# Optimization experiments

Hardware: AMD Instinct MI355X
Metric: run time of the kernel (lower is better)

Reference implementation:

```python
import jax, jax.numpy as jnp
import numpy as np

N_HEADS = 16
HEAD_DIM = 64
STRIDE = 32  # default local_attention_ctx used as stride in 'strided' mode


def _strided_fill_mask(n):
    # Faithful to the torch code: positions where (i >= j) and ((i - j) % stride == 0)
    # get mask value 1, and the code does masked_fill_(mask == 1, -inf),
    # i.e. those positions are set to -inf (inverted polarity, replicated as-is).
    i = jnp.arange(n)[:, None]
    j = jnp.arange(n)[None, :]
    return (i >= j) & (((i - j) % STRIDE) == 0)  # [n, n] bool, True -> -inf


def setup_inputs() -> dict:
    key = jax.random.key(0)
    k_x, k_qkv, k_out = jax.random.split(key, 3)
    b, n, c = 2, 2048, 1024
    inner = N_HEADS * HEAD_DIM  # 1024
    x = jax.random.normal(k_x, (b, n, c), dtype=jnp.float32)
    W_qkv = jax.random.normal(k_qkv, (c, 3 * inner), dtype=jnp.float32) * 0.02
    W_out = jax.random.normal(k_out, (inner, c), dtype=jnp.float32) * 0.02
    b_out = jnp.zeros((c,), dtype=jnp.float32)
    return {"x": x, "W_qkv": W_qkv, "W_out": W_out, "b_out": b_out}


def reference(x, W_qkv, W_out, b_out):
    b, n, c = x.shape
    h, hd = N_HEADS, HEAD_DIM
    scale = c ** (-0.5)  # n_embeddings ** -0.5, as in the original

    qkv = x @ W_qkv                              # [b, n, 3*h*hd]
    q, k, v = jnp.split(qkv, 3, axis=-1)
    def to_heads(t):
        return t.reshape(b, n, h, hd).transpose(0, 2, 1, 3)  # [b, h, n, hd]
    q, k, v = to_heads(q), to_heads(k), to_heads(v)

    dots = jnp.einsum('bhid,bhjd->bhij', q, k) * scale       # [b, h, n, n]
    fill = _strided_fill_mask(n)                             # [n, n]
    dots = jnp.where(fill[None, None], -jnp.inf, dots)

    attn = jax.nn.softmax(dots, axis=-1)
    out = jnp.einsum('bhij,bhjd->bhid', attn, v)             # [b, h, n, hd]
    out = out.transpose(0, 2, 1, 3).reshape(b, n, h * hd)    # [b, n, inner]
    out = out @ W_out + b_out                                # dropout: eval/identity
    return out
```

## Files before the change

kernel.cpp:

```cpp
#include <hip/hip_runtime.h>

typedef __attribute__((ext_vector_type(8))) short bf16x8;
typedef __attribute__((ext_vector_type(4))) float f32x4;

#if __has_builtin(__builtin_amdgcn_exp2f)
#define EXP2F(x) __builtin_amdgcn_exp2f(x)
#else
extern "C" __device__ float __ocml_native_exp2_f32(float);
#define EXP2F(x) __ocml_native_exp2_f32(x)
#endif

#define QSCALE 0.04508422002778011f
#define NS 2048

__device__ __forceinline__ ushort f32_to_bf16(float f) {
  union { float f; unsigned u; } x; x.f = f;
  unsigned r = x.u + 0x7fffu + ((x.u >> 16) & 1u);
  return (ushort)(r >> 16);
}

__device__ __forceinline__ unsigned pack_bf16(float f0, float f1) {
#if __has_builtin(__builtin_amdgcn_cvt_pk_bf16_f32)
  auto pr = __builtin_amdgcn_cvt_pk_bf16_f32(f0, f1);
  unsigned u; __builtin_memcpy(&u, &pr, sizeof(u)); return u;
#else
  union { float f; unsigned u; } a, b;
  a.f = f0; b.f = f1;
  return __builtin_amdgcn_perm(b.u + 0x8000u, a.u + 0x8000u, 0x07060302u);
#endif
}

__device__ __forceinline__ void load16_to_lds(const void* g, void* l) {
  __builtin_amdgcn_global_load_lds(
      (const __attribute__((address_space(1))) unsigned int*)(
          reinterpret_cast<uintptr_t>(g)),
      (__attribute__((address_space(3))) unsigned int*)(
          reinterpret_cast<uintptr_t>(l)),
      16, 0, 0);
}

__global__ __launch_bounds__(256) void prep(
    const float* __restrict__ x, const float* __restrict__ Wqkv,
    ushort* __restrict__ xb, ushort* __restrict__ wqkvT)
{
  __shared__ ushort tile[32][33];
  const int bid = blockIdx.x, t = threadIdx.x;
  if (bid < 2048) {
    size_t i = (size_t)bid * 256 + t;
    const float4* p = (const float4*)(x + i * 8);
    float4 a = p[0], b = p[1];
    union { uint4 v; ushort s[8]; } u;
    u.s[0] = f32_to_bf16(a.x); u.s[1] = f32_to_bf16(a.y);
    u.s[2] = f32_to_bf16(a.z); u.s[3] = f32_to_bf16(a.w);
    u.s[4] = f32_to_bf16(b.x); u.s[5] = f32_to_bf16(b.y);
    u.s[6] = f32_to_bf16(b.z); u.s[7] = f32_to_bf16(b.w);
    *(uint4*)(xb + i * 8) = u.v;
  } else {
    int tb = bid - 2048;
    int cb = (tb % 96) * 32, rb = (tb / 96) * 32;
    int tx = t & 31, ty = t >> 5;
    float s = (cb + tx) < 1024 ? QSCALE : 1.0f;
#pragma unroll
    for (int k = 0; k < 4; ++k)
      tile[ty + 8 * k][tx] =
          f32_to_bf16(Wqkv[(size_t)(rb + ty + 8 * k) * 3072 + cb + tx] * s);
    __syncthreads();
#pragma unroll
    for (int k = 0; k < 4; ++k)
      wqkvT[(size_t)(cb + ty + 8 * k) * 1024 + rb + tx] = tile[tx][ty + 8 * k];
  }
}

__global__ __launch_bounds__(256) void transpose_w(
    const float* __restrict__ in, ushort* __restrict__ out, int R, int C)
{
  __shared__ ushort tile[32][33];
  int t = threadIdx.x, tx = t & 31, ty = t >> 5;
  int rb = blockIdx.y * 32, cb = blockIdx.x * 32;
#pragma unroll
  for (int k = 0; k < 4; ++k)
    tile[ty + 8 * k][tx] = f32_to_bf16(in[(size_t)(rb + ty + 8 * k) * C + cb + tx]);
  __syncthreads();
#pragma unroll
  for (int k = 0; k < 4; ++k)
    out[(size_t)(cb + ty + 8 * k) * R + rb + tx] = tile[tx][ty + 8 * k];
}

template <typename TC>
__device__ __forceinline__ void gemm_core(
    const ushort* __restrict__ A, const ushort* __restrict__ Bt,
    const float* __restrict__ bias, TC* __restrict__ C,
    int N, int K, int mbase, int nbase,
    ushort* __restrict__ sA0, ushort* __restrict__ sB0,
    ushort* __restrict__ sA1, ushort* __restrict__ sB1)
{
  const int t = threadIdx.x;
  const int lane = t & 63, w = t >> 6;
  const int quad = lane >> 4, l16 = lane & 15;
  const int wr = w >> 1, wc = w & 1;
  const int lrow = lane >> 2, lchunk = (lane & 3) * 8;

  f32x4 acc[4][4];
#pragma unroll
  for (int i = 0; i < 4; ++i)
#pragma unroll
    for (int j = 0; j < 4; ++j)
      acc[i][j] = (f32x4){0.f, 0.f, 0.f, 0.f};

#pragma unroll
  for (int r = 0; r < 2; ++r) {
    int rb = w * 32 + r * 16;
    load16_to_lds(&A[(size_t)(mbase + rb + lrow) * K + lchunk], &sA0[rb * 32]);
    load16_to_lds(&Bt[(size_t)(nbase + rb + lrow) * K + lchunk], &sB0[rb * 32]);
  }

  for (int kb = 0; kb < K; kb += 32) {
    const bool odd = (kb >> 5) & 1;
    ushort* sA = odd ? sA1 : sA0;
    ushort* sB = odd ? sB1 : sB0;
    ushort* pA = odd ? sA0 : sA1;
    ushort* pB = odd ? sB0 : sB1;
    __syncthreads();
    if (kb + 32 < K) {
#pragma unroll
      for (int r = 0; r < 2; ++r) {
        int rb = w * 32 + r * 16;
        load16_to_lds(&A[(size_t)(mbase + rb + lrow) * K + kb + 32 + lchunk],
                      &pA[rb * 32]);
        load16_to_lds(&Bt[(size_t)(nbase + rb + lrow) * K + kb + 32 + lchunk],
                      &pB[rb * 32]);
      }
    }

    bf16x8 af[4], bf[4];
#pragma unroll
    for (int mt = 0; mt < 4; ++mt)
      af[mt] = *(const bf16x8*)&sA[(wr * 64 + mt * 16 + l16) * 32 + quad * 8];
#pragma unroll
    for (int nt = 0; nt < 4; ++nt)
      bf[nt] = *(const bf16x8*)&sB[(wc * 64 + nt * 16 + l16) * 32 + quad * 8];
#pragma unroll
    for (int mt = 0; mt < 4; ++mt)
#pragma unroll
      for (int nt = 0; nt < 4; ++nt)
        acc[mt][nt] = __builtin_amdgcn_mfma_f32_16x16x32_bf16(
            af[mt], bf[nt], acc[mt][nt], 0, 0, 0);
  }

#pragma unroll
  for (int mt = 0; mt < 4; ++mt) {
#pragma unroll
    for (int nt = 0; nt < 4; ++nt) {
      int col = nbase + wc * 64 + nt * 16 + l16;
      float bv = bias ? bias[col] : 0.f;
#pragma unroll
      for (int ri = 0; ri < 4; ++ri) {
        int row = mbase + wr * 64 + mt * 16 + quad * 4 + ri;
        float val = acc[mt][nt][ri] + bv;
        if constexpr (__is_same(TC, float))
          C[(size_t)row * N + col] = val;
        else
          C[(size_t)row * N + col] = f32_to_bf16(val);
      }
    }
  }
}

__global__ __launch_bounds__(256) void gemm_qkvt(
    const ushort* __restrict__ xb, const ushort* __restrict__ wqkvT,
    ushort* __restrict__ qk, ushort* __restrict__ vtbuf)
{
  __shared__ ushort sA0[128 * 32], sB0[128 * 32];
  __shared__ ushort sA1[128 * 32], sB1[128 * 32];
  const int bid = blockIdx.x;
  if (bid < 512) {
    gemm_core<ushort>(xb, wqkvT, nullptr, qk, 2048, 1024,
                      (bid >> 4) * 128, (bid & 15) * 128, sA0, sB0, sA1, sB1);
  } else {
    const int id = bid - 512;
    gemm_core<ushort>(wqkvT + (size_t)2048 * 1024, xb, nullptr, vtbuf,
                      4096, 1024, (id >> 5) * 128, (id & 31) * 128,
                      sA0, sB0, sA1, sB1);
  }
}

__global__ __launch_bounds__(256) void gemm_out(
    const ushort* __restrict__ attnb, const ushort* __restrict__ woutT,
    const float* __restrict__ bias, float* __restrict__ out)
{
  __shared__ ushort sA0[128 * 32], sB0[128 * 32];
  __shared__ ushort sA1[128 * 32], sB1[128 * 32];
  const int bid = blockIdx.x;
  gemm_core<float>(attnb, woutT, bias, out, 1024, 1024,
                   (bid >> 3) * 128, (bid & 7) * 128, sA0, sB0, sA1, sB1);
}

__device__ __forceinline__ void stage_kv(
    const ushort* __restrict__ qk, const ushort* __restrict__ vt,
    ushort* sKb, ushort* sVb, int b, int h, int kvbase,
    int w, int rowK, int csw)
{
#pragma unroll
  for (int g = 0; g < 2; ++g) {
    int rk = w * 16 + g * 8 + rowK;
    load16_to_lds(&qk[((size_t)(b * NS + kvbase + rk)) * 2048 + 1024 + h * 64 + csw],
                  &sKb[(w * 16 + g * 8) * 64]);
    load16_to_lds(&vt[((size_t)(h * 64 + rk)) * 4096 + b * 2048 + kvbase + csw],
                  &sVb[(w * 16 + g * 8) * 64]);
  }
}

__global__ __launch_bounds__(256) void attn_kernel(
    const ushort* __restrict__ qk, const ushort* __restrict__ vt,
    ushort* __restrict__ attn_out)
{
  __shared__ ushort sK[2][64 * 64];
  __shared__ ushort sV[2][64 * 64];
  __shared__ ushort sPt[4][32][72];

  const int t = threadIdx.x;
  const int lane = t & 63, w = t >> 6;
  const int quad = lane >> 4, l16 = lane & 15;
  const int bh = blockIdx.y, b = bh >> 4, h = bh & 15;
  const int qbase = blockIdx.x * 128;
  const int rowK = lane >> 3;
  const int csw = ((lane & 7) ^ rowK) * 8;
  const int swz = l16 & 7;

  bf16x8 qf[2][2];
#pragma unroll
  for (int is = 0; is < 2; ++is)
#pragma unroll
    for (int c = 0; c < 2; ++c)
      qf[is][c] = *(const bf16x8*)&qk[
          ((size_t)(b * NS + qbase + w * 32 + is * 16 + l16)) * 2048 +
          h * 64 + c * 32 + quad * 8];

  bf16x8 ones;
  { union { bf16x8 v; ushort s[8]; } ou;
#pragma unroll
    for (int i = 0; i < 8; ++i) ou.s[i] = 0x3F80;
    ones = ou.v; }

  unsigned amask[2][4][2];
#pragma unroll
  for (int is = 0; is < 2; ++is)
#pragma unroll
    for (int mt = 0; mt < 4; ++mt)
#pragma unroll
      for (int hf = 0; hf < 2; ++hf) {
        int r0 = hf * 2, r1 = hf * 2 + 1;
        int base = is * 16 + l16 - mt * 16 - quad * 4;
        unsigned m = 0xFFFFFFFFu;
        if (((base - r0) & 31) == 0) m &= 0xFFFF0000u;
        if (((base - r1) & 31) == 0) m &= 0x0000FFFFu;
        amask[is][mt][hf] = m;
      }

  const int ib64 = (qbase + w * 32) >> 6;

  f32x4 oacc[2][4];
#pragma unroll
  for (int is = 0; is < 2; ++is)
#pragma unroll
    for (int dt = 0; dt < 4; ++dt) oacc[is][dt] = (f32x4){0.f, 0.f, 0.f, 0.f};
  f32x4 lsum[2];
  lsum[0] = (f32x4){0.f, 0.f, 0.f, 0.f};
  lsum[1] = (f32x4){0.f, 0.f, 0.f, 0.f};

  stage_kv(qk, vt, sK[0], sV[0], b, h, 0, w, rowK, csw);

  for (int kb = 0; kb < NS / 64; ++kb) {
    const int cur = kb & 1;
    const int kvbase = kb * 64;
    __syncthreads();
    if (kb < NS / 64 - 1)
      stage_kv(qk, vt, sK[cur ^ 1], sV[cur ^ 1], b, h, kvbase + 64, w, rowK, csw);

    const ushort* K = sK[cur];
    const ushort* V = sV[cur];

    f32x4 st[2][4];
#pragma unroll
    for (int is = 0; is < 2; ++is)
#pragma unroll
      for (int mt = 0; mt < 4; ++mt) st[is][mt] = (f32x4){0.f, 0.f, 0.f, 0.f};
#pragma unroll
    for (int mt = 0; mt < 4; ++mt)
#pragma unroll
      for (int c = 0; c < 2; ++c) {
        bf16x8 kf = *(const bf16x8*)&K[(mt * 16 + l16) * 64 +
                                       (((c * 4 + quad) ^ swz) * 8)];
        st[0][mt] = __builtin_amdgcn_mfma_f32_16x16x32_bf16(
            kf, qf[0][c], st[0][mt], 0, 0, 0);
        st[1][mt] = __builtin_amdgcn_mfma_f32_16x16x32_bf16(
            kf, qf[1][c], st[1][mt], 0, 0, 0);
      }

    if (kb < ib64) {
#pragma unroll
      for (int is = 0; is < 2; ++is)
#pragma unroll
        for (int mt = 0; mt < 4; ++mt) {
          unsigned lo = pack_bf16(EXP2F(st[is][mt][0]), EXP2F(st[is][mt][1])) &
                        amask[is][mt][0];
          unsigned hi = pack_bf16(EXP2F(st[is][mt][2]), EXP2F(st[is][mt][3])) &
                        amask[is][mt][1];
          *(uint2*)&sPt[w][is * 16 + l16][mt * 16 + quad * 4] =
              make_uint2(lo, hi);
        }
    } else if (kb > ib64) {
#pragma unroll
      for (int is = 0; is < 2; ++is)
#pragma unroll
        for (int mt = 0; mt < 4; ++mt) {
          unsigned lo = pack_bf16(EXP2F(st[is][mt][0]), EXP2F(st[is][mt][1]));
          unsigned hi = pack_bf16(EXP2F(st[is][mt][2]), EXP2F(st[is][mt][3]));
          *(uint2*)&sPt[w][is * 16 + l16][mt * 16 + quad * 4] =
              make_uint2(lo, hi);
        }
    } else {
#pragma unroll
      for (int is = 0; is < 2; ++is) {
        int irow = qbase + w * 32 + is * 16 + l16;
#pragma unroll
        for (int mt = 0; mt < 4; ++mt) {
          float p[4];
#pragma unroll
          for (int ri = 0; ri < 4; ++ri) {
            int j = kvbase + mt * 16 + quad * 4 + ri;
            p[ri] = EXP2F(st[is][mt][ri]);
            unsigned du = (unsigned)(irow - j);
            if ((du & 0x8000001Fu) == 0u) p[ri] = 0.f;
          }
          unsigned lo = pack_bf16(p[0], p[1]);
          unsigned hi = pack_bf16(p[2], p[3]);
          *(uint2*)&sPt[w][is * 16 + l16][mt * 16 + quad * 4] =
              make_uint2(lo, hi);
        }
      }
    }

#pragma unroll
    for (int c2 = 0; c2 < 2; ++c2) {
      bf16x8 vf[4];
#pragma unroll
      for (int dt = 0; dt < 4; ++dt)
        vf[dt] = *(const bf16x8*)&V[(dt * 16 + l16) * 64 +
                                    (((c2 * 4 + quad) ^ swz) * 8)];
#pragma unroll
      for (int is = 0; is < 2; ++is) {
        bf16x8 pf = *(const bf16x8*)&sPt[w][is * 16 + l16][c2 * 32 + quad * 8];
        lsum[is] = __builtin_amdgcn_mfma_f32_16x16x32_bf16(
            pf, ones, lsum[is], 0, 0, 0);
#pragma unroll
        for (int dt = 0; dt < 4; ++dt)
          oacc[is][dt] = __builtin_amdgcn_mfma_f32_16x16x32_bf16(
              pf, vf[dt], oacc[is][dt], 0, 0, 0);
      }
    }
  }

#pragma unroll
  for (int is = 0; is < 2; ++is)
#pragma unroll
    for (int ri = 0; ri < 4; ++ri) {
      float inv = __builtin_amdgcn_rcpf(lsum[is][ri]);
      int ig = qbase + w * 32 + is * 16 + quad * 4 + ri;
#pragma unroll
      for (int dt = 0; dt < 4; ++dt)
        attn_out[(size_t)(b * NS + ig) * 1024 + h * 64 + dt * 16 + l16] =
            f32_to_bf16(oacc[is][dt][ri] * inv);
    }
}

extern "C" void kernel_launch(void* const* d_in, const int* in_sizes, int n_in,
                              void* d_out, int out_size, void* d_ws, size_t ws_size,
                              hipStream_t stream) {
  const float* x    = (const float*)d_in[0];
  const float* Wqkv = (const float*)d_in[1];
  const float* Wout = (const float*)d_in[2];
  const float* bout = (const float*)d_in[3];
  float* out = (float*)d_out;

  ushort* qk    = (ushort*)d_ws;
  ushort* vt    = qk + (size_t)4096 * 2048;
  ushort* xb    = vt + (size_t)1024 * 4096;
  ushort* wqkvT = xb + (size_t)4096 * 1024;
  ushort* attnb = xb;
  ushort* woutT = wqkvT;

  prep<<<2048 + 3072, 256, 0, stream>>>(x, Wqkv, xb, wqkvT);
  gemm_qkvt<<<768, 256, 0, stream>>>(xb, wqkvT, qk, vt);
  transpose_w<<<dim3(32, 32), 256, 0, stream>>>(Wout, woutT, 1024, 1024);
  attn_kernel<<<dim3(NS / 128, 32), 256, 0, stream>>>(qk, vt, attnb);
  gemm_out<<<256, 256, 0, stream>>>(attnb, woutT, bout, out);
}
```

Measured before the change: 196.1 us.

## Fuse Wout transpose into prep, swizzle GEMM LDS, retile output GEMM

Folds the W_out bf16 transpose into the prep kernel, removing one launch and giving woutT its own workspace slot. Adds an XOR swizzle on the LDS layout in the shared GEMM core to reduce bank conflicts on fragment reads. Retiles the output GEMM to 64x128 tiles with BK=64, launching 512 blocks instead of 256 for better CU fill. It also drops the hardware packed bf16 convert in favour of a perm-based path, which may alter rounding in attention.

Result: faster. 188.3 us (-4.0%).

```diff
diff --git a/kernel.cpp b/kernel.cpp
--- a/kernel.cpp
+++ b/kernel.cpp
@@ -20,14 +20,9 @@
 }
 
 __device__ __forceinline__ unsigned pack_bf16(float f0, float f1) {
-#if __has_builtin(__builtin_amdgcn_cvt_pk_bf16_f32)
-  auto pr = __builtin_amdgcn_cvt_pk_bf16_f32(f0, f1);
-  unsigned u; __builtin_memcpy(&u, &pr, sizeof(u)); return u;
-#else
   union { float f; unsigned u; } a, b;
   a.f = f0; b.f = f1;
   return __builtin_amdgcn_perm(b.u + 0x8000u, a.u + 0x8000u, 0x07060302u);
-#endif
 }
 
 __device__ __forceinline__ void load16_to_lds(const void* g, void* l) {
@@ -41,7 +36,9 @@
 
 __global__ __launch_bounds__(256) void prep(
     const float* __restrict__ x, const float* __restrict__ Wqkv,
-    ushort* __restrict__ xb, ushort* __restrict__ wqkvT)
+    const float* __restrict__ Wout,
+    ushort* __restrict__ xb, ushort* __restrict__ wqkvT,
+    ushort* __restrict__ woutT)
 {
   __shared__ ushort tile[32][33];
   const int bid = blockIdx.x, t = threadIdx.x;
@@ -55,7 +52,7 @@
     u.s[4] = f32_to_bf16(b.x); u.s[5] = f32_to_bf16(b.y);
     u.s[6] = f32_to_bf16(b.z); u.s[7] = f32_to_bf16(b.w);
     *(uint4*)(xb + i * 8) = u.v;
-  } else {
+  } else if (bid < 5120) {
     int tb = bid - 2048;
     int cb = (tb % 96) * 32, rb = (tb / 96) * 32;
     int tx = t & 31, ty = t >> 5;
@@ -68,25 +65,42 @@
 #pragma unroll
     for (int k = 0; k < 4; ++k)
       wqkvT[(size_t)(cb + ty + 8 * k) * 1024 + rb + tx] = tile[tx][ty + 8 * k];
-  }
-}
-
-__global__ __launch_bounds__(256) void transpose_w(
-    const float* __restrict__ in, ushort* __restrict__ out, int R, int C)
-{
-  __shared__ ushort tile[32][33];
-  int t = threadIdx.x, tx = t & 31, ty = t >> 5;
-  int rb = blockIdx.y * 32, cb = blockIdx.x * 32;
-#pragma unroll
-  for (int k = 0; k < 4; ++k)
-    tile[ty + 8 * k][tx] = f32_to_bf16(in[(size_t)(rb + ty + 8 * k) * C + cb + tx]);
-  __syncthreads();
-#pragma unroll
-  for (int k = 0; k < 4; ++k)
-    out[(size_t)(cb + ty + 8 * k) * R + rb + tx] = tile[tx][ty + 8 * k];
-}
-
-template <typename TC>
+  } else {
+    int tb = bid - 5120;
+    int cb = (tb & 31) * 32, rb = (tb >> 5) * 32;
+    int tx = t & 31, ty = t >> 5;
+#pragma unroll
+    for (int k = 0; k < 4; ++k)
+      tile[ty + 8 * k][tx] =
+          f32_to_bf16(Wout[(size_t)(rb + ty + 8 * k) * 1024 + cb + tx]);
+    __syncthreads();
+#pragma unroll
+    for (int k = 0; k < 4; ++k)
+      woutT[(size_t)(cb + ty + 8 * k) * 1024 + rb + tx] = tile[tx][ty + 8 * k];
+  }
+}
+
+template <int TM, int BK>
+__device__ __forceinline__ void stage_ab(
+    const ushort* __restrict__ A, const ushort* __restrict__ Bt,
+    int K, int mbase, int nbase, int kb,
+    ushort* __restrict__ sA, ushort* __restrict__ sB,
+    int w, int lrow, int gofs)
+{
+  constexpr int ROWS = (BK == 32) ? 16 : 8;
+#pragma unroll
+  for (int r = 0; r < TM / (ROWS * 4); ++r) {
+    int rb = w * (TM / 4) + r * ROWS;
+    load16_to_lds(&A[(size_t)(mbase + rb + lrow) * K + kb + gofs], &sA[rb * BK]);
+  }
+#pragma unroll
+  for (int r = 0; r < 128 / (ROWS * 4); ++r) {
+    int rb = w * 32 + r * ROWS;
+    load16_to_lds(&Bt[(size_t)(nbase + rb + lrow) * K + kb + gofs], &sB[rb * BK]);
+  }
+}
+
+template <int TM, int BK, typename TC>
 __device__ __forceinline__ void gemm_core(
     const ushort* __restrict__ A, const ushort* __restrict__ Bt,
     const float* __restrict__ bias, TC* __restrict__ C,
@@ -94,68 +108,65 @@
     ushort* __restrict__ sA0, ushort* __restrict__ sB0,
     ushort* __restrict__ sA1, ushort* __restrict__ sB1)
 {
+  constexpr int MT = TM / 32;
   const int t = threadIdx.x;
   const int lane = t & 63, w = t >> 6;
   const int quad = lane >> 4, l16 = lane & 15;
   const int wr = w >> 1, wc = w & 1;
-  const int lrow = lane >> 2, lchunk = (lane & 3) * 8;
-
-  f32x4 acc[4][4];
-#pragma unroll
-  for (int i = 0; i < 4; ++i)
+  const int lrow = (BK == 32) ? (lane >> 2) : (lane >> 3);
+  const int gofs = (BK == 32)
+      ? (((lane & 3) ^ ((lane >> 3) & 3)) * 8)
+      : (((lane & 7) ^ (lane >> 3)) * 8);
+  const int rswz = (BK == 32) ? ((l16 >> 1) & 3) : (l16 & 7);
+
+  f32x4 acc[MT][4];
+#pragma unroll
+  for (int i = 0; i < MT; ++i)
 #pragma unroll
     for (int j = 0; j < 4; ++j)
       acc[i][j] = (f32x4){0.f, 0.f, 0.f, 0.f};
 
-#pragma unroll
-  for (int r = 0; r < 2; ++r) {
-    int rb = w * 32 + r * 16;
-    load16_to_lds(&A[(size_t)(mbase + rb + lrow) * K + lchunk], &sA0[rb * 32]);
-    load16_to_lds(&Bt[(size_t)(nbase + rb + lrow) * K + lchunk], &sB0[rb * 32]);
-  }
-
-  for (int kb = 0; kb < K; kb += 32) {
-    const bool odd = (kb >> 5) & 1;
+  stage_ab<TM, BK>(A, Bt, K, mbase, nbase, 0, sA0, sB0, w, lrow, gofs);
+
+  for (int kb = 0; kb < K; kb += BK) {
+    const bool odd = (kb / BK) & 1;
     ushort* sA = odd ? sA1 : sA0;
     ushort* sB = odd ? sB1 : sB0;
     ushort* pA = odd ? sA0 : sA1;
     ushort* pB = odd ? sB0 : sB1;
     __syncthreads();
-    if (kb + 32 < K) {
-#pragma unroll
-      for (int r = 0; r < 2; ++r) {
-        int rb = w * 32 + r * 16;
-        load16_to_lds(&A[(size_t)(mbase + rb + lrow) * K + kb + 32 + lchunk],
-                      &pA[rb * 32]);
-        load16_to_lds(&Bt[(size_t)(nbase + rb + lrow) * K + kb + 32 + lchunk],
-                      &pB[rb * 32]);
-      }
+    if (kb + BK < K)
+      stage_ab<TM, BK>(A, Bt, K, mbase, nbase, kb + BK, pA, pB, w, lrow, gofs);
+
+#pragma unroll
+    for (int c = 0; c < BK / 32; ++c) {
+      bf16x8 af[MT], bfr[4];
+#pragma unroll
+      for (int mt = 0; mt < MT; ++mt)
+        af[mt] = *(const bf16x8*)&sA[(wr * (TM / 2) + mt * 16 + l16) * BK +
+                                     (((c * 4 + quad) ^ rswz) * 8)];
+#pragma unroll
+      for (int nt = 0; nt < 4; ++nt)
+        bfr[nt] = *(const bf16x8*)&sB[(wc * 64 + nt * 16 + l16) * BK +
+                                      (((c * 4 + quad) ^ rswz) * 8)];
+#pragma unroll
+      for (int mt = 0; mt < MT; ++mt)
+#pragma unroll
+        for (int nt = 0; nt < 4; ++nt)
+          acc[mt][nt] = __builtin_amdgcn_mfma_f32_16x16x32_bf16(
+              af[mt], bfr[nt], acc[mt][nt], 0, 0, 0);
     }
-
-    bf16x8 af[4], bf[4];
-#pragma unroll
-    for (int mt = 0; mt < 4; ++mt)
-      af[mt] = *(const bf16x8*)&sA[(wr * 64 + mt * 16 + l16) * 32 + quad * 8];
-#pragma unroll
-    for (int nt = 0; nt < 4; ++nt)
-      bf[nt] = *(const bf16x8*)&sB[(wc * 64 + nt * 16 + l16) * 32 + quad * 8];
-#pragma unroll
-    for (int mt = 0; mt < 4; ++mt)
-#pragma unroll
-      for (int nt = 0; nt < 4; ++nt)
-        acc[mt][nt] = __builtin_amdgcn_mfma_f32_16x16x32_bf16(
-            af[mt], bf[nt], acc[mt][nt], 0, 0, 0);
-  }
-
-#pragma unroll
-  for (int mt = 0; mt < 4; ++mt) {
+  }
+
+#pragma unroll
+  for (int mt = 0; mt < MT; ++mt) {
 #pragma unroll
     for (int nt = 0; nt < 4; ++nt) {
       int col = nbase + wc * 64 + nt * 16 + l16;
       float bv = bias ? bias[col] : 0.f;
 #pragma unroll
       for (int ri = 0; ri < 4; ++ri) {
-        int row = mbase + wr * 64 + mt * 16 + quad * 4 + ri;
+        int row = mbase + wr * (TM / 2) + mt * 16 + quad * 4 + ri;
         float val = acc[mt][nt][ri] + bv;
         if constexpr (__is_same(TC, float))
           C[(size_t)row * N + col] = val;
@@ -174,13 +185,14 @@
   __shared__ ushort sA1[128 * 32], sB1[128 * 32];
   const int bid = blockIdx.x;
   if (bid < 512) {
-    gemm_core<ushort>(xb, wqkvT, nullptr, qk, 2048, 1024,
-                      (bid >> 4) * 128, (bid & 15) * 128, sA0, sB0, sA1, sB1);
+    gemm_core<128, 32, ushort>(xb, wqkvT, nullptr, qk, 2048, 1024,
+                               (bid >> 4) * 128, (bid & 15) * 128,
+                               sA0, sB0, sA1, sB1);
   } else {
     const int id = bid - 512;
-    gemm_core<ushort>(wqkvT + (size_t)2048 * 1024, xb, nullptr, vtbuf,
-                      4096, 1024, (id >> 5) * 128, (id & 31) * 128,
-                      sA0, sB0, sA1, sB1);
+    gemm_core<128, 32, ushort>(wqkvT + (size_t)2048 * 1024, xb, nullptr, vtbuf,
+                               4096, 1024, (id >> 5) * 128, (id & 31) * 128,
+                               sA0, sB0, sA1, sB1);
   }
 }
 
@@ -188,11 +200,12 @@
     const ushort* __restrict__ attnb, const ushort* __restrict__ woutT,
     const float* __restrict__ bias, float* __restrict__ out)
 {
-  __shared__ ushort sA0[128 * 32], sB0[128 * 32];
-  __shared__ ushort sA1[128 * 32], sB1[128 * 32];
+  __shared__ ushort sA0[64 * 64], sB0[128 * 64];
+  __shared__ ushort sA1[64 * 64], sB1[128 * 64];
   const int bid = blockIdx.x;
-  gemm_core<float>(attnb, woutT, bias, out, 1024, 1024,
-                   (bid >> 3) * 128, (bid & 7) * 128, sA0, sB0, sA1, sB1);
+  gemm_core<64, 64, float>(attnb, woutT, bias, out, 1024, 1024,
+                           (bid >> 3) * 64, (bid & 7) * 128,
+                           sA0, sB0, sA1, sB1);
 }
 
 __device__ __forceinline__ void stage_kv(
@@ -387,12 +400,11 @@
   ushort* vt    = qk + (size_t)4096 * 2048;
   ushort* xb    = vt + (size_t)1024 * 4096;
   ushort* wqkvT = xb + (size_t)4096 * 1024;
+  ushort* woutT = wqkvT + (size_t)3072 * 1024;
   ushort* attnb = xb;
-  ushort* woutT = wqkvT;
-
-  prep<<<2048 + 3072, 256, 0, stream>>>(x, Wqkv, xb, wqkvT);
+
+  prep<<<6144, 256, 0, stream>>>(x, Wqkv, Wout, xb, wqkvT, woutT);
   gemm_qkvt<<<768, 256, 0, stream>>>(xb, wqkvT, qk, vt);
-  transpose_w<<<dim3(32, 32), 256, 0, stream>>>(Wout, woutT, 1024, 1024);
   attn_kernel<<<dim3(NS / 128, 32), 256, 0, stream>>>(qk, vt, attnb);
-  gemm_out<<<256, 256, 0, stream>>>(attnb, woutT, bout, out);
-}
+  gemm_out<<<512, 256, 0, stream>>>(attnb, woutT, bout, out);
+}
```
